# Kernel tuning notes

Measured on AMD Instinct MI355X. Metric: run time of the kernel, lower is better.

## Reference

```python
import jax, jax.numpy as jnp
import numpy as np

B, H, S, D = 8, 16, 1024, 128


def setup_inputs() -> dict:
    key = jax.random.key(0)
    kq, kk, kv = jax.random.split(key, 3)
    queries = jax.random.normal(kq, (B, H, S, D), dtype=jnp.float32)
    keys = jax.random.normal(kk, (B, H, S, D), dtype=jnp.float32)
    values = jax.random.normal(kv, (B, H, S, D), dtype=jnp.float32)
    # learnable per-element scale over the full score tensor, init 'ones'
    scale = jnp.ones((B, H, S, S), dtype=jnp.float32)
    return {"queries": queries, "keys": keys, "values": values, "scale": scale}


def reference(queries, keys, values, scale):
    # scores: [B,H,Sq,Sk] = Q K^T
    scores = jnp.einsum("bhqd,bhkd->bhqk", queries, keys)
    # custom learnable scaling: scores / sqrt(scale[0]) * scale
    # scale[0] has shape [H,Sq,Sk] and broadcasts over the batch dim
    scores = scores / jnp.sqrt(scale[0]) * scale
    # masked_softmax with attention_mask=None -> plain softmax over keys axis
    attn = jax.nn.softmax(scores, axis=-1)
    # dropout is identity (rate 0 / eval mode)
    out = jnp.einsum("bhqk,bhkd->bhqd", attn, values)
    return out
```

## Files before the change

kernel.cpp:

```cpp
#include <hip/hip_runtime.h>
#include <math.h>

#define NB 8
#define NH 16
#define NS 1024
#define ND 128

#define BN 32
#define NT (NS / BN)
#define TILE_SH (BN * ND)
#define PSTR 40

typedef float    f32x4 __attribute__((ext_vector_type(4)));
typedef _Float16 f16x8 __attribute__((ext_vector_type(8)));
typedef _Float16 f16x4 __attribute__((ext_vector_type(4)));

#define MFMAH(a, b, c) __builtin_amdgcn_mfma_f32_16x16x32_f16(a, b, c, 0, 0, 0)

__device__ __forceinline__ void gload16(const void* g, void* l) {
  __builtin_amdgcn_global_load_lds(
      (const __attribute__((address_space(1))) void*)g,
      (__attribute__((address_space(3))) void*)l, 16, 0, 0);
}

__global__ void prep_all(const float* __restrict__ scale, _Float16* __restrict__ E,
                         const float* __restrict__ K, short* __restrict__ Kimg,
                         const float* __restrict__ V, short* __restrict__ Vimg,
                         int base) {
  __shared__ _Float16 tbuf[BN * 132];
  const int x = blockIdx.x + base;
  const int tid = threadIdx.x;
  if (x < 8192) {
    const size_t i0 = ((size_t)x * 256 + tid) * 8;
    float4 a0 = *(const float4*)(scale + i0);
    float4 b0 = *(const float4*)(scale + i0 + 4);
    float r[8] = {rsqrtf(a0.x), rsqrtf(a0.y), rsqrtf(a0.z), rsqrtf(a0.w),
                  rsqrtf(b0.x), rsqrtf(b0.y), rsqrtf(b0.z), rsqrtf(b0.w)};
    *(f16x8*)(E + i0) =
        (f16x8){(_Float16)(a0.x * r[0]), (_Float16)(a0.y * r[1]),
                (_Float16)(a0.z * r[2]), (_Float16)(a0.w * r[3]),
                (_Float16)(b0.x * r[4]), (_Float16)(b0.y * r[5]),
                (_Float16)(b0.z * r[6]), (_Float16)(b0.w * r[7])};
#pragma unroll
    for (int b = 1; b < NB; ++b) {
      const float* sp = scale + ((size_t)b << 24) + i0;
      float4 a = *(const float4*)sp;
      float4 bb = *(const float4*)(sp + 4);
      *(f16x8*)(E + ((size_t)b << 24) + i0) =
          (f16x8){(_Float16)(a.x * r[0]),  (_Float16)(a.y * r[1]),
                  (_Float16)(a.z * r[2]),  (_Float16)(a.w * r[3]),
                  (_Float16)(bb.x * r[4]), (_Float16)(bb.y * r[5]),
                  (_Float16)(bb.z * r[6]), (_Float16)(bb.w * r[7])};
    }
  } else if (x < 12288) {
    const int p = x - 8192;
    const int t = p & 31, bh = p >> 5;
    const float* Kt = K + ((size_t)bh * NS + t * BN) * ND;
    short* img = Kimg + ((size_t)bh * NT + t) * TILE_SH;
#pragma unroll
    for (int i = 0; i < 4; ++i) {
      int f = tid + i * 256;
      int key = f >> 5, d4 = (f & 31) << 2;
      float4 v = *(const float4*)(Kt + (size_t)key * ND + d4);
      f16x4 hv = {(_Float16)v.x, (_Float16)v.y, (_Float16)v.z, (_Float16)v.w};
      int gp = (d4 >> 3) ^ (key & 15);
      *(f16x4*)(img + key * 128 + gp * 8 + (d4 & 7)) = hv;
    }
  } else {
    const int p = x - 12288;
    const int t = p & 31, bh = p >> 5;
    const float* Vt = V + ((size_t)bh * NS + t * BN) * ND;
#pragma unroll
    for (int i = 0; i < 4; ++i) {
      int f = tid + i * 256;
      int key = f >> 5, d4 = (f & 31) << 2;
      float4 v = *(const float4*)(Vt + (size_t)key * ND + d4);
      *(f16x4*)&tbuf[key * 132 + d4] =
          (f16x4){(_Float16)v.x, (_Float16)v.y, (_Float16)v.z, (_Float16)v.w};
    }
    __syncthreads();
    short* img = Vimg + ((size_t)bh * NT + t) * TILE_SH;
#pragma unroll
    for (int i = 0; i < 2; ++i) {
      int u = tid + i * 256;
      int d = u >> 2, k8 = u & 3;
      f16x8 o;
#pragma unroll
      for (int e = 0; e < 8; ++e) o[e] = tbuf[(k8 * 8 + e) * 132 + d];
      *(f16x8*)(img + d * BN + ((k8 ^ ((d >> 1) & 3)) * 8)) = o;
    }
  }
}


#define ISSUE(T, B)                                              \
  do {                                                           \
    const short* kg_ = Kb + (T) * TILE_SH + tid * 8;             \
    const short* vg_ = Vb + (T) * TILE_SH + tid * 8;             \
    gload16(kg_, &Ks[B][tid * 8]);                               \
    gload16(kg_ + 2048, &Ks[B][tid * 8 + 2048]);                 \
    gload16(vg_, &Vs[B][tid * 8]);                               \
    gload16(vg_ + 2048, &Vs[B][tid * 8 + 2048]);                 \
  } while (0)

#define LOADE(DST, T)                                                             \
  do {                                                                            \
    _Pragma("unroll") for (int nf = 0; nf < 2; ++nf)                              \
        _Pragma("unroll") for (int m0 = 0; m0 < 2; ++m0)                          \
            DST[nf][m0] = *(const f16x4*)(Eb + (size_t)(q0 + nf * 16 + c) * NS +  \
                                          (T) * BN + m0 * 16 + quad * 4);         \
  } while (0)

#define LOADS(SV, S0, T)                                                          \
  do {                                                                            \
    _Pragma("unroll") for (int nf = 0; nf < 2; ++nf)                              \
        _Pragma("unroll") for (int m0 = 0; m0 < 2; ++m0) {                        \
      size_t off_ = (size_t)(q0 + nf * 16 + c) * NS + (T) * BN + m0 * 16 + quad * 4; \
      SV[nf][m0] = *(const f32x4*)(sclb + off_);                                  \
      S0[nf][m0] = *(const f32x4*)(sc0b + off_);                                  \
    }                                                                             \
  } while (0)

#define TILE_STEP(BUF, EF, SCV, SC0, KT)                                             \
  do {                                                                               \
    f32x4 S_[2][2];                                                                  \
    _Pragma("unroll") for (int nf = 0; nf < 2; ++nf)                                 \
        _Pragma("unroll") for (int m0 = 0; m0 < 2; ++m0)                             \
            S_[nf][m0] = (f32x4){0.f, 0.f, 0.f, 0.f};                                \
    _Pragma("unroll") for (int m0 = 0; m0 < 2; ++m0) {                               \
      _Pragma("unroll") for (int kb = 0; kb < 4; ++kb) {                             \
        const f16x8 a_ = *(const f16x8*)&Ks[BUF][(m0 * 16 + c) * 128 +               \
                                                 (((kb << 2) | quad) ^ c) * 8];      \
        S_[0][m0] = MFMAH(a_, qf[0][kb], S_[0][m0]);                                 \
        S_[1][m0] = MFMAH(a_, qf[1][kb], S_[1][m0]);                                 \
      }                                                                              \
    }                                                                                \
    float al2_[2];                                                                   \
    int skipall_ = 1;                                                                \
    _Pragma("unroll") for (int nf = 0; nf < 2; ++nf) {                               \
      float sv[8];                                                                   \
      _Pragma("unroll") for (int m0 = 0; m0 < 2; ++m0)                               \
          _Pragma("unroll") for (int r = 0; r < 4; ++r) {                            \
        float e_ = USE_E ? (float)EF[nf][m0][r]                                      \
                         : SCV[nf][m0][r] * rsqrtf(SC0[nf][m0][r]);                  \
        sv[m0 * 4 + r] = S_[nf][m0][r] * e_;                                         \
      }                                                                              \
      float tm = sv[0];                                                              \
      _Pragma("unroll") for (int i = 1; i < 8; ++i) tm = fmaxf(tm, sv[i]);           \
      tm = fmaxf(tm, __shfl_xor(tm, 16));                                            \
      tm = fmaxf(tm, __shfl_xor(tm, 32));                                            \
      float mn, al;                                                                  \
      if (__all(tm <= m_[nf])) {                         \
        mn = m_[nf]; al = 1.f;                                                       \
      } else {                                                                       \
        mn = fmaxf(m_[nf], tm);                                                      \
        al = __expf(m_[nf] - mn);                                                    \
        m_[nf] = mn;                                                                 \
        skipall_ = 0;                                                                \
      }                                                                              \
      al2_[nf] = al;                                                                 \
      float ps = 0.f;                                                                \
      _Float16 pb[8];                                                                \
      _Pragma("unroll") for (int i = 0; i < 8; ++i) {                                \
        float p_ = __expf(sv[i] - mn);                                               \
        ps += p_;                                                                    \
        pb[i] = (_Float16)p_;                                                        \
      }                                                                              \
      ps += __shfl_xor(ps, 16);                                                      \
      ps += __shfl_xor(ps, 32);                                                      \
      ls_[nf] = ls_[nf] * al + ps;                                                   \
      _Float16* pr_ = &Ps[(size_t)(w * 32 + nf * 16 + c) * PSTR];                    \
      *(f16x4*)(pr_ + quad * 4)      = (f16x4){pb[0], pb[1], pb[2], pb[3]};          \
      *(f16x4*)(pr_ + 16 + quad * 4) = (f16x4){pb[4], pb[5], pb[6], pb[7]};          \
    }                                                                                \
    if (!skipall_) {                                                                 \
      _Pragma("unroll") for (int pf = 0; pf < 2; ++pf) {                             \
        float ar_[4];                                                                \
        _Pragma("unroll") for (int r = 0; r < 4; ++r)                                \
            ar_[r] = __shfl(al2_[pf], quad * 4 + r);                                 \
        _Pragma("unroll") for (int n0 = 0; n0 < 8; ++n0)                             \
            _Pragma("unroll") for (int r = 0; r < 4; ++r) O[pf][n0][r] *= ar_[r];    \
      }                                                                              \
    }                                                                                \
    const f16x8 pf0_ = *(const f16x8*)&Ps[(size_t)(w * 32 + c) * PSTR + quad * 8];   \
    const f16x8 pf1_ =                                                               \
        *(const f16x8*)&Ps[(size_t)(w * 32 + 16 + c) * PSTR + quad * 8];             \
    _Pragma("unroll") for (int n0 = 0; n0 < 8; ++n0) {                               \
      const f16x8 b_ = *(const f16x8*)&Vs[BUF][(n0 * 16 + c) * 32 +                  \
                                              (quad ^ ((c >> 1) & 3)) * 8];          \
      O[0][n0] = MFMAH(pf0_, b_, O[0][n0]);                                          \
      O[1][n0] = MFMAH(pf1_, b_, O[1][n0]);                                          \
    }                                                                                \
  } while (0)

template <bool USE_E>
__launch_bounds__(256, 3)
__global__ void attn_f16(const float* __restrict__ Q, const short* __restrict__ Kimg,
                         const short* __restrict__ Vimg, const _Float16* __restrict__ E,
                         const float* __restrict__ scale, float* __restrict__ out) {
  __shared__ short Ks[2][TILE_SH];
  __shared__ short Vs[2][TILE_SH];
  __shared__ _Float16 Ps[128 * PSTR];

  const int tid = threadIdx.x;
  const int w = tid >> 6, l = tid & 63;
  const int quad = l >> 4, c = l & 15;

  const int x = blockIdx.x;
  const int bh = ((x >> 6) << 3) | (x & 7);
  const int qblk = (x >> 3) & 7;
  const int q0 = qblk * 128 + w * 32;

  const short* Kb = Kimg + (size_t)bh * (NT * TILE_SH);
  const short* Vb = Vimg + (size_t)bh * (NT * TILE_SH);
  const _Float16* Eb = E + ((size_t)bh << 20);
  const float* sclb = scale + ((size_t)bh << 20);
  const float* sc0b = scale + ((size_t)(bh & 15) << 20);

  ISSUE(0, 0);
  f16x4 efA[2][2], efB[2][2];
  if (USE_E) LOADE(efA, 0);

  f16x8 qf[2][4];
  {
    const float* Qb = Q + ((size_t)bh * NS + q0) * ND;
#pragma unroll
    for (int nf = 0; nf < 2; ++nf)
#pragma unroll
      for (int kb = 0; kb < 4; ++kb) {
        const float* p = Qb + (size_t)(nf * 16 + c) * ND + kb * 32 + quad * 8;
        float4 a = *(const float4*)p;
        float4 b = *(const float4*)(p + 4);
        qf[nf][kb] = (f16x8){(_Float16)a.x, (_Float16)a.y, (_Float16)a.z, (_Float16)a.w,
                             (_Float16)b.x, (_Float16)b.y, (_Float16)b.z, (_Float16)b.w};
      }
  }

  float m_[2] = {-INFINITY, -INFINITY}, ls_[2] = {0.f, 0.f};
  f32x4 O[2][8];
#pragma unroll
  for (int pf = 0; pf < 2; ++pf)
#pragma unroll
    for (int n0 = 0; n0 < 8; ++n0) O[pf][n0] = (f32x4){0.f, 0.f, 0.f, 0.f};

  f32x4 sclvA[2][2], sc0vA[2][2], sclvB[2][2], sc0vB[2][2];

#pragma unroll 1
  for (int kt = 0; kt < NT; kt += 2) {
    __syncthreads();
    if (!USE_E) LOADS(sclvA, sc0vA, kt);
    ISSUE(kt + 1, 1);
    if (USE_E) LOADE(efB, kt + 1);
    TILE_STEP(0, efA, sclvA, sc0vA, kt);
    __syncthreads();
    if (!USE_E) LOADS(sclvB, sc0vB, kt + 1);
    if (kt + 2 < NT) {
      ISSUE(kt + 2, 0);
      if (USE_E) LOADE(efA, kt + 2);
    }
    TILE_STEP(1, efB, sclvB, sc0vB, kt + 1);
  }

  float* ob = out + ((size_t)bh * NS + q0) * ND;
#pragma unroll
  for (int pf = 0; pf < 2; ++pf)
#pragma unroll
    for (int r = 0; r < 4; ++r) {
      float lv = __shfl(ls_[pf], quad * 4 + r);
      float inv = 1.0f / lv;
      int row = pf * 16 + quad * 4 + r;
#pragma unroll
      for (int n0 = 0; n0 < 8; ++n0)
        ob[(size_t)row * ND + n0 * 16 + c] = O[pf][n0][r] * inv;
    }
}

#define TQ 16
#define TK 64
#define PITCH 129
__launch_bounds__(256, 2)
__global__ void attn_fp32(const float* __restrict__ Q, const float* __restrict__ K,
                          const float* __restrict__ V, const float* __restrict__ scale,
                          float* __restrict__ out) {
  __shared__ float qs[TQ][ND];
  __shared__ float kv[TK][PITCH];
  __shared__ float ps[4][4][TK];
  const int tid = threadIdx.x;
  const int w = tid >> 6, l = tid & 63;
  const int bid = blockIdx.x;
  const int qt = bid & 63, h = (bid >> 6) & 15, b = bid >> 10;
  const size_t bh = (size_t)b * NH + h;
  const float* Qb = Q + (bh * NS + (size_t)qt * TQ) * ND;
  const float* Kb = K + bh * NS * ND;
  const float* Vb = V + bh * NS * ND;
  {
    const float4* Q4 = (const float4*)Qb;
    float4* qs4 = (float4*)&qs[0][0];
    qs4[tid] = Q4[tid];
    qs4[tid + 256] = Q4[tid + 256];
  }
  const int q0 = qt * TQ + w * 4;
  const float* sc0p[4];
  const float* sclp[4];
#pragma unroll
  for (int i = 0; i < 4; ++i) {
    const int qg = q0 + i;
    sc0p[i] = scale + ((size_t)h * NS + qg) * NS;
    sclp[i] = scale + (bh * NS + qg) * NS;
  }
  float m[4] = {-INFINITY, -INFINITY, -INFINITY, -INFINITY};
  float lsum[4] = {0.f, 0.f, 0.f, 0.f};
  float oa[4] = {0.f, 0.f, 0.f, 0.f};
  float ob[4] = {0.f, 0.f, 0.f, 0.f};
  for (int kt = 0; kt < NS / TK; ++kt) {
    __syncthreads();
    {
      const float4* K4 = (const float4*)(Kb + (size_t)kt * TK * ND);
#pragma unroll
      for (int i = 0; i < 8; ++i) {
        const int f = tid + i * 256;
        const float4 t4 = K4[f];
        const int r = f >> 5, cc = (f & 31) << 2;
        kv[r][cc] = t4.x; kv[r][cc + 1] = t4.y; kv[r][cc + 2] = t4.z; kv[r][cc + 3] = t4.w;
      }
    }
    __syncthreads();
    const int kg = kt * TK + l;
    float sc0[4], scl[4];
#pragma unroll
    for (int i = 0; i < 4; ++i) { sc0[i] = sc0p[i][kg]; scl[i] = sclp[i][kg]; }
    float s[4] = {0.f, 0.f, 0.f, 0.f};
#pragma unroll 8
    for (int d = 0; d < ND; ++d) {
      const float kd = kv[l][d];
      s[0] = fmaf(qs[w * 4 + 0][d], kd, s[0]);
      s[1] = fmaf(qs[w * 4 + 1][d], kd, s[1]);
      s[2] = fmaf(qs[w * 4 + 2][d], kd, s[2]);
      s[3] = fmaf(qs[w * 4 + 3][d], kd, s[3]);
    }
#pragma unroll
    for (int i = 0; i < 4; ++i) {
      const float svv = s[i] * scl[i] * rsqrtf(sc0[i]);
      float mx = svv;
#pragma unroll
      for (int off = 32; off > 0; off >>= 1) mx = fmaxf(mx, __shfl_xor(mx, off));
      const float mn = fmaxf(m[i], mx);
      const float p = __expf(svv - mn);
      const float al = __expf(m[i] - mn);
      float psum = p;
#pragma unroll
      for (int off = 32; off > 0; off >>= 1) psum += __shfl_xor(psum, off);
      lsum[i] = lsum[i] * al + psum;
      m[i] = mn;
      oa[i] *= al;
      ob[i] *= al;
      ps[w][i][l] = p;
    }
    __syncthreads();
    {
      const float4* V4 = (const float4*)(Vb + (size_t)kt * TK * ND);
#pragma unroll
      for (int i = 0; i < 8; ++i) {
        const int f = tid + i * 256;
        const float4 t4 = V4[f];
        const int r = f >> 5, cc = (f & 31) << 2;
        kv[r][cc] = t4.x; kv[r][cc + 1] = t4.y; kv[r][cc + 2] = t4.z; kv[r][cc + 3] = t4.w;
      }
    }
    __syncthreads();
#pragma unroll 4
    for (int k2 = 0; k2 < TK; ++k2) {
      const float v0 = kv[k2][l];
      const float v1 = kv[k2][64 + l];
#pragma unroll
      for (int i = 0; i < 4; ++i) {
        const float p = ps[w][i][k2];
        oa[i] = fmaf(p, v0, oa[i]);
        ob[i] = fmaf(p, v1, ob[i]);
      }
    }
  }
  float* op = out + (bh * NS + q0) * ND;
#pragma unroll
  for (int i = 0; i < 4; ++i) {
    const float inv = 1.0f / lsum[i];
    op[(size_t)i * ND + l] = oa[i] * inv;
    op[(size_t)i * ND + 64 + l] = ob[i] * inv;
  }
}

extern "C" void kernel_launch(void* const* d_in, const int* in_sizes, int n_in,
                              void* d_out, int out_size, void* d_ws, size_t ws_size,
                              hipStream_t stream) {
  const float* Q = (const float*)d_in[0];
  const float* K = (const float*)d_in[1];
  const float* V = (const float*)d_in[2];
  const float* scale = (const float*)d_in[3];
  float* out = (float*)d_out;

  const size_t KV_BYTES = (size_t)NB * NH * NS * ND * 2;
  const size_t E_BYTES = (size_t)NB * NH * NS * NS * 2;
  const size_t needB = 2 * KV_BYTES;
  const size_t needA = needB + E_BYTES;

  if (ws_size >= needB) {
    short* Kimg = (short*)d_ws;
    short* Vimg = (short*)((char*)d_ws + KV_BYTES);
    if (ws_size >= needA) {
      _Float16* E = (_Float16*)((char*)d_ws + needB);
      prep_all<<<dim3(16384), dim3(256), 0, stream>>>(scale, E, K, Kimg, V, Vimg, 0);
      attn_f16<true><<<dim3(1024), dim3(256), 0, stream>>>(Q, Kimg, Vimg, E, scale, out);
    } else {
      prep_all<<<dim3(8192), dim3(256), 0, stream>>>(scale, nullptr, K, Kimg, V, Vimg,
                                                     8192);
      attn_f16<false><<<dim3(1024), dim3(256), 0, stream>>>(Q, Kimg, Vimg, nullptr,
                                                            scale, out);
    }
  } else {
    attn_fp32<<<dim3(NB * NH * (NS / TK) * 4), dim3(256), 0, stream>>>(Q, K, V, scale,
                                                                       out);
  }
}
```

Measured before the change: 1.013 ms.

## Drop precomputed fp16 scale tensor; stream scale directly with one-tile prefetch

```diff
diff --git a/kernel.cpp b/kernel.cpp
--- a/kernel.cpp
+++ b/kernel.cpp
@@ -23,38 +23,13 @@
       (__attribute__((address_space(3))) void*)l, 16, 0, 0);
 }
 
-__global__ void prep_all(const float* __restrict__ scale, _Float16* __restrict__ E,
-                         const float* __restrict__ K, short* __restrict__ Kimg,
-                         const float* __restrict__ V, short* __restrict__ Vimg,
-                         int base) {
+__global__ void prep_kv(const float* __restrict__ K, short* __restrict__ Kimg,
+                        const float* __restrict__ V, short* __restrict__ Vimg) {
   __shared__ _Float16 tbuf[BN * 132];
-  const int x = blockIdx.x + base;
+  const int x = blockIdx.x;
   const int tid = threadIdx.x;
-  if (x < 8192) {
-    const size_t i0 = ((size_t)x * 256 + tid) * 8;
-    float4 a0 = *(const float4*)(scale + i0);
-    float4 b0 = *(const float4*)(scale + i0 + 4);
-    float r[8] = {rsqrtf(a0.x), rsqrtf(a0.y), rsqrtf(a0.z), rsqrtf(a0.w),
-                  rsqrtf(b0.x), rsqrtf(b0.y), rsqrtf(b0.z), rsqrtf(b0.w)};
-    *(f16x8*)(E + i0) =
-        (f16x8){(_Float16)(a0.x * r[0]), (_Float16)(a0.y * r[1]),
-                (_Float16)(a0.z * r[2]), (_Float16)(a0.w * r[3]),
-                (_Float16)(b0.x * r[4]), (_Float16)(b0.y * r[5]),
-                (_Float16)(b0.z * r[6]), (_Float16)(b0.w * r[7])};
-#pragma unroll
-    for (int b = 1; b < NB; ++b) {
-      const float* sp = scale + ((size_t)b << 24) + i0;
-      float4 a = *(const float4*)sp;
-      float4 bb = *(const float4*)(sp + 4);
-      *(f16x8*)(E + ((size_t)b << 24) + i0) =
-          (f16x8){(_Float16)(a.x * r[0]),  (_Float16)(a.y * r[1]),
-                  (_Float16)(a.z * r[2]),  (_Float16)(a.w * r[3]),
-                  (_Float16)(bb.x * r[4]), (_Float16)(bb.y * r[5]),
-                  (_Float16)(bb.z * r[6]), (_Float16)(bb.w * r[7])};
-    }
-  } else if (x < 12288) {
-    const int p = x - 8192;
-    const int t = p & 31, bh = p >> 5;
+  if (x < 4096) {
+    const int t = x & 31, bh = x >> 5;
     const float* Kt = K + ((size_t)bh * NS + t * BN) * ND;
     short* img = Kimg + ((size_t)bh * NT + t) * TILE_SH;
 #pragma unroll
@@ -67,7 +42,7 @@
       *(f16x4*)(img + key * 128 + gp * 8 + (d4 & 7)) = hv;
     }
   } else {
-    const int p = x - 12288;
+    const int p = x - 4096;
     const int t = p & 31, bh = p >> 5;
     const float* Vt = V + ((size_t)bh * NS + t * BN) * ND;
 #pragma unroll
@@ -103,25 +78,17 @@
     gload16(vg_ + 2048, &Vs[B][tid * 8 + 2048]);                 \
   } while (0)
 
-#define LOADE(DST, T)                                                             \
-  do {                                                                            \
-    _Pragma("unroll") for (int nf = 0; nf < 2; ++nf)                              \
-        _Pragma("unroll") for (int m0 = 0; m0 < 2; ++m0)                          \
-            DST[nf][m0] = *(const f16x4*)(Eb + (size_t)(q0 + nf * 16 + c) * NS +  \
-                                          (T) * BN + m0 * 16 + quad * 4);         \
+#define LOADS(SV, S0, T)                                                             \
+  do {                                                                               \
+    _Pragma("unroll") for (int nf = 0; nf < 2; ++nf)                                 \
+        _Pragma("unroll") for (int m0 = 0; m0 < 2; ++m0) {                           \
+      size_t off_ = (size_t)(q0 + nf * 16 + c) * NS + (T) * BN + m0 * 16 + quad * 4; \
+      SV[nf][m0] = *(const f32x4*)(sclb + off_);                                     \
+      S0[nf][m0] = *(const f32x4*)(sc0b + off_);                                     \
+    }                                                                                \
   } while (0)
 
-#define LOADS(SV, S0, T)                                                          \
-  do {                                                                            \
-    _Pragma("unroll") for (int nf = 0; nf < 2; ++nf)                              \
-        _Pragma("unroll") for (int m0 = 0; m0 < 2; ++m0) {                        \
-      size_t off_ = (size_t)(q0 + nf * 16 + c) * NS + (T) * BN + m0 * 16 + quad * 4; \
-      SV[nf][m0] = *(const f32x4*)(sclb + off_);                                  \
-      S0[nf][m0] = *(const f32x4*)(sc0b + off_);                                  \
-    }                                                                             \
-  } while (0)
-
-#define TILE_STEP(BUF, EF, SCV, SC0, KT)                                             \
+#define TILE_STEP(BUF, SCV, SC0)                                                     \
   do {                                                                               \
     f32x4 S_[2][2];                                                                  \
     _Pragma("unroll") for (int nf = 0; nf < 2; ++nf)                                 \
@@ -141,8 +108,7 @@
       float sv[8];                                                                   \
       _Pragma("unroll") for (int m0 = 0; m0 < 2; ++m0)                               \
           _Pragma("unroll") for (int r = 0; r < 4; ++r) {                            \
-        float e_ = USE_E ? (float)EF[nf][m0][r]                                      \
-                         : SCV[nf][m0][r] * rsqrtf(SC0[nf][m0][r]);                  \
+        float e_ = SCV[nf][m0][r] * rsqrtf(SC0[nf][m0][r]);                          \
         sv[m0 * 4 + r] = S_[nf][m0][r] * e_;                                         \
       }                                                                              \
       float tm = sv[0];                                                              \
@@ -193,11 +159,10 @@
     }                                                                                \
   } while (0)
 
-template <bool USE_E>
-__launch_bounds__(256, 3)
+__launch_bounds__(256, 2)
 __global__ void attn_f16(const float* __restrict__ Q, const short* __restrict__ Kimg,
-                         const short* __restrict__ Vimg, const _Float16* __restrict__ E,
-                         const float* __restrict__ scale, float* __restrict__ out) {
+                         const short* __restrict__ Vimg, const float* __restrict__ scale,
+                         float* __restrict__ out) {
   __shared__ short Ks[2][TILE_SH];
   __shared__ short Vs[2][TILE_SH];
   __shared__ _Float16 Ps[128 * PSTR];
@@ -213,24 +178,29 @@
 
   const short* Kb = Kimg + (size_t)bh * (NT * TILE_SH);
   const short* Vb = Vimg + (size_t)bh * (NT * TILE_SH);
-  const _Float16* Eb = E + ((size_t)bh << 20);
   const float* sclb = scale + ((size_t)bh << 20);
   const float* sc0b = scale + ((size_t)(bh & 15) << 20);
 
-  ISSUE(0, 0);
-  f16x4 efA[2][2], efB[2][2];
-  if (USE_E) LOADE(efA, 0);
-
   f16x8 qf[2][4];
+  f32x4 sclvA[2][2], sc0vA[2][2], sclvB[2][2], sc0vB[2][2];
   {
     const float* Qb = Q + ((size_t)bh * NS + q0) * ND;
+    float4 qa[2][4][2];
 #pragma unroll
     for (int nf = 0; nf < 2; ++nf)
 #pragma unroll
       for (int kb = 0; kb < 4; ++kb) {
         const float* p = Qb + (size_t)(nf * 16 + c) * ND + kb * 32 + quad * 8;
-        float4 a = *(const float4*)p;
-        float4 b = *(const float4*)(p + 4);
+        qa[nf][kb][0] = *(const float4*)p;
+        qa[nf][kb][1] = *(const float4*)(p + 4);
+      }
+    ISSUE(0, 0);
+    LOADS(sclvA, sc0vA, 0);
+#pragma unroll
+    for (int nf = 0; nf < 2; ++nf)
+#pragma unroll
+      for (int kb = 0; kb < 4; ++kb) {
+        float4 a = qa[nf][kb][0], b = qa[nf][kb][1];
         qf[nf][kb] = (f16x8){(_Float16)a.x, (_Float16)a.y, (_Float16)a.z, (_Float16)a.w,
                              (_Float16)b.x, (_Float16)b.y, (_Float16)b.z, (_Float16)b.w};
       }
@@ -243,22 +213,18 @@
 #pragma unroll
     for (int n0 = 0; n0 < 8; ++n0) O[pf][n0] = (f32x4){0.f, 0.f, 0.f, 0.f};
 
-  f32x4 sclvA[2][2], sc0vA[2][2], sclvB[2][2], sc0vB[2][2];
-
 #pragma unroll 1
   for (int kt = 0; kt < NT; kt += 2) {
     __syncthreads();
-    if (!USE_E) LOADS(sclvA, sc0vA, kt);
     ISSUE(kt + 1, 1);
-    if (USE_E) LOADE(efB, kt + 1);
-    TILE_STEP(0, efA, sclvA, sc0vA, kt);
-    __syncthreads();
-    if (!USE_E) LOADS(sclvB, sc0vB, kt + 1);
+    LOADS(sclvB, sc0vB, kt + 1);
+    TILE_STEP(0, sclvA, sc0vA);
+    __syncthreads();
     if (kt + 2 < NT) {
       ISSUE(kt + 2, 0);
-      if (USE_E) LOADE(efA, kt + 2);
-    }
-    TILE_STEP(1, efB, sclvB, sc0vB, kt + 1);
+      LOADS(sclvA, sc0vA, kt + 2);
+    }
+    TILE_STEP(1, sclvB, sc0vB);
   }
 
   float* ob = out + ((size_t)bh * NS + q0) * ND;
@@ -399,23 +365,13 @@
   float* out = (float*)d_out;
 
   const size_t KV_BYTES = (size_t)NB * NH * NS * ND * 2;
-  const size_t E_BYTES = (size_t)NB * NH * NS * NS * 2;
   const size_t needB = 2 * KV_BYTES;
-  const size_t needA = needB + E_BYTES;
 
   if (ws_size >= needB) {
     short* Kimg = (short*)d_ws;
     short* Vimg = (short*)((char*)d_ws + KV_BYTES);
-    if (ws_size >= needA) {
-      _Float16* E = (_Float16*)((char*)d_ws + needB);
-      prep_all<<<dim3(16384), dim3(256), 0, stream>>>(scale, E, K, Kimg, V, Vimg, 0);
-      attn_f16<true><<<dim3(1024), dim3(256), 0, stream>>>(Q, Kimg, Vimg, E, scale, out);
-    } else {
-      prep_all<<<dim3(8192), dim3(256), 0, stream>>>(scale, nullptr, K, Kimg, V, Vimg,
-                                                     8192);
-      attn_f16<false><<<dim3(1024), dim3(256), 0, stream>>>(Q, Kimg, Vimg, nullptr,
-                                                            scale, out);
-    }
+    prep_kv<<<dim3(8192), dim3(256), 0, stream>>>(K, Kimg, V, Vimg);
+    attn_f16<<<dim3(1024), dim3(256), 0, stream>>>(Q, Kimg, Vimg, scale, out);
   } else {
     attn_fp32<<<dim3(NB * NH * (NS / TK) * 4), dim3(256), 0, stream>>>(Q, K, V, scale,
                                                                        out);
```

Result: faster. 922.5 us (-8.9%).
